# Kernel tuning notes

Measured on AMD Instinct MI355X. Metric: run time of the kernel, lower is better.

The kernel has to match this reference:

```python
import jax, jax.numpy as jnp
import numpy as np

NUM_HEADS = 16
NUM_KV_HEADS = 4
HEAD_DIM = 128
WINDOW = 1024  # sliding window: key j visible to query i iff 0 <= i - j <= WINDOW
SCALE = 0.08838834764831845  # 1/sqrt(HEAD_DIM)
NEG_INF = -1e30


def setup_inputs() -> dict:
    key = jax.random.key(0)
    k1, k2, k3, k4 = jax.random.split(key, 4)
    B, S = 4, 2048
    T = B * S
    return {
        "q": jax.random.normal(k1, (T, NUM_HEADS * HEAD_DIM), dtype=jnp.float32),
        "k": jax.random.normal(k2, (T, NUM_KV_HEADS * HEAD_DIM), dtype=jnp.float32),
        "v": jax.random.normal(k3, (T, NUM_KV_HEADS * HEAD_DIM), dtype=jnp.float32),
        "sinks": jax.random.normal(k4, (NUM_HEADS,), dtype=jnp.float32),
        "batch": B,
        "seqlen": S,
    }


def reference(q, k, v, sinks, batch, seqlen):
    """Varlen causal sliding-window attention with learnable per-head sink logits.

    Equal-length sequences: total_tokens = batch * seqlen, matching
    cu_seqlens = [0, S, 2S, ...] in flash_attn_varlen_func.
    """
    B, S = batch, seqlen
    g = NUM_HEADS // NUM_KV_HEADS
    q = q.reshape(B, S, NUM_HEADS, HEAD_DIM)
    k = k.reshape(B, S, NUM_KV_HEADS, HEAD_DIM)
    v = v.reshape(B, S, NUM_KV_HEADS, HEAD_DIM)
    # GQA: expand kv heads to match query heads
    k = jnp.repeat(k, g, axis=2)  # [B,S,H,D]
    v = jnp.repeat(v, g, axis=2)

    logits = jnp.einsum("bqhd,bkhd->bhqk", q, k) * SCALE  # [B,H,S,S]

    i = jnp.arange(S)[:, None]
    j = jnp.arange(S)[None, :]
    mask = (j <= i) & ((i - j) <= WINDOW)  # causal + sliding window (left=WINDOW, right=-1)
    logits = jnp.where(mask, logits, NEG_INF)

    # Learnable sink: one extra virtual logit per head, contributing no value.
    sink_col = jnp.broadcast_to(sinks[None, :, None, None], (B, NUM_HEADS, S, 1))
    logits = jnp.concatenate([logits, sink_col], axis=-1)  # [B,H,S,S+1]
    probs = jax.nn.softmax(logits, axis=-1)[..., :S]  # drop sink prob (value = 0)

    o = jnp.einsum("bhqk,bkhd->bqhd", probs, v)  # [B,S,H,D]
    return o.reshape(B * S, NUM_HEADS * HEAD_DIM)
```

## Files before the change

### kernel.cpp

```cpp
#include <hip/hip_runtime.h>
#include <hip/hip_bf16.h>

#define NH    16
#define NKVH  4
#define HD    128
#define WIN   1024
#define SEQ   2048
#define NB    4
#define QROW  (NH * HD)
#define KROW  (NKVH * HD)
#define LOG2E 1.4426950408889634f
#define QSC   (0.08838834764831845f * LOG2E)
#define DTHR  8.0f

#define KSTR 136
#define VSTR 40

typedef __attribute__((ext_vector_type(8))) short short8;
typedef __attribute__((ext_vector_type(4))) float float4v;

__device__ __forceinline__ unsigned short f2bf(float f) {
    unsigned int u = __float_as_uint(f);
    unsigned int r = (u + 0x7FFFu + ((u >> 16) & 1u)) >> 16;
    return (unsigned short)r;
}

__device__ __forceinline__ unsigned int pk2bf(float a, float b) {
    float2 t; t.x = a; t.y = b;
    __hip_bfloat162 h = __float22bfloat162_rn(t);
    union { __hip_bfloat162 h; unsigned int u; } cv;
    cv.h = h;
    return cv.u;
}

__global__ __launch_bounds__(256)
void cvt_k_kernel(const float* __restrict__ kg, unsigned short* __restrict__ kb) {
    const size_t idx = ((size_t)blockIdx.x * 256 + threadIdx.x) * 8;
    float4 a = *(const float4*)(kg + idx);
    float4 b = *(const float4*)(kg + idx + 4);
    uint4 w;
    w.x = pk2bf(a.x, a.y); w.y = pk2bf(a.z, a.w);
    w.z = pk2bf(b.x, b.y); w.w = pk2bf(b.z, b.w);
    *(uint4*)(kb + idx) = w;
}

#define VTSTR 72
__global__ __launch_bounds__(256)
void cvt_vt_kernel(const float* __restrict__ vg, unsigned short* __restrict__ vt) {
    __shared__ unsigned short T[128 * VTSTR];
    const int blk = blockIdx.x;
    const int b   = blk >> 7;
    const int kvh = (blk >> 5) & 3;
    const int kb  = blk & 31;
    const int t   = threadIdx.x;

    const int klocal = t >> 2;
    const int d0     = (t & 3) * 32;
    const float* src = vg + (size_t)(b * SEQ + kb * 64 + klocal) * KROW + kvh * HD + d0;
#pragma unroll
    for (int c = 0; c < 8; ++c) {
        float4 x = *(const float4*)(src + c * 4);
        T[(d0 + c * 4 + 0) * VTSTR + klocal] = f2bf(x.x);
        T[(d0 + c * 4 + 1) * VTSTR + klocal] = f2bf(x.y);
        T[(d0 + c * 4 + 2) * VTSTR + klocal] = f2bf(x.z);
        T[(d0 + c * 4 + 3) * VTSTR + klocal] = f2bf(x.w);
    }
    __syncthreads();

    const int d    = t >> 1;
    const int half = t & 1;
    const unsigned short* s = &T[d * VTSTR + half * 32];
    unsigned short* dst = vt + ((size_t)((b * NKVH + kvh) * HD) + d) * SEQ + kb * 64 + half * 32;
#pragma unroll
    for (int c = 0; c < 4; ++c)
        *(uint4*)(dst + c * 8) = *(const uint4*)(s + c * 8);
}

__global__ __launch_bounds__(256, 3)
void attn_swa_sink_kernel(const float* __restrict__ qg,
                          const unsigned short* __restrict__ kb,
                          const unsigned short* __restrict__ vt,
                          const float* __restrict__ sinks,
                          float* __restrict__ og) {
    __shared__ __align__(16) unsigned short Klds[2][32 * KSTR];
    __shared__ __align__(16) unsigned short Vlds[2][128 * VSTR];

    const int gid  = blockIdx.x;
    const int xcd  = gid & 7;
    const int rest = gid >> 3;
    const int qt   = 63 - (rest >> 1);
    const int g    = ((rest & 1) << 3) | xcd;
    const int b    = g >> 2;
    const int kvh  = g & 3;

    const int tid  = threadIdx.x;
    const int wave = tid >> 6;
    const int lane = tid & 63;
    const int l15  = lane & 15;
    const int quad = lane >> 4;
    const int h    = kvh * 4 + wave;
    const int q0   = qt * 32;

    const float* qbase = qg + (size_t)(b * SEQ) * QROW;
    const unsigned short* kbase = kb + (size_t)(b * SEQ) * KROW + kvh * HD;
    const unsigned short* vtbase = vt + (size_t)((b * NKVH + kvh) * HD) * SEQ;

    short8 qf[2][4];
#pragma unroll
    for (int qs = 0; qs < 2; ++qs) {
        const float* qr = qbase + (size_t)(q0 + qs * 16 + l15) * QROW + h * HD + quad * 8;
#pragma unroll
        for (int c = 0; c < 4; ++c) {
            float4 x = *(const float4*)(qr + c * 32);
            float4 y = *(const float4*)(qr + c * 32 + 4);
            union { unsigned int u[4]; short8 s; } cv;
            cv.u[0] = pk2bf(x.x * QSC, x.y * QSC);
            cv.u[1] = pk2bf(x.z * QSC, x.w * QSC);
            cv.u[2] = pk2bf(y.x * QSC, y.y * QSC);
            cv.u[3] = pk2bf(y.z * QSC, y.w * QSC);
            qf[qs][c] = cv.s;
        }
    }

    const float sinkv = sinks[h] * LOG2E;
    float m_i[2] = { sinkv, sinkv };
    float l_i[2] = { 0.0f, 0.0f };
    float4v accO[2][8];
#pragma unroll
    for (int qs = 0; qs < 2; ++qs)
#pragma unroll
        for (int f = 0; f < 8; ++f) accO[qs][f] = (float4v)0.0f;

    const int kr  = tid >> 3, kcg = tid & 7;
    const int lrow = ((kr & 1) << 4) | (kr >> 1);
    const int vd  = tid >> 1, vh = tid & 1;

    int kt0 = q0 - WIN; if (kt0 < 0) kt0 = 0;
    const int kend = q0 + 32;

    const int koff = lrow * KSTR + kcg * 16;
    const int voff = vd * VSTR + vh * 16;

    uint4 kpre0, kpre1, vpre0, vpre1;
    {
        const unsigned short* kp = kbase + (size_t)(kt0 + kr) * KROW + kcg * 16;
        kpre0 = *(const uint4*)(kp);
        kpre1 = *(const uint4*)(kp + 8);
        const unsigned short* vp = vtbase + (size_t)vd * SEQ + kt0 + vh * 16;
        vpre0 = *(const uint4*)(vp);
        vpre1 = *(const uint4*)(vp + 8);
    }

    int pp = 0;
    for (int k0 = kt0; k0 < kend; k0 += 32, pp ^= 1) {
        *(uint4*)&Klds[pp][koff]     = kpre0;
        *(uint4*)&Klds[pp][koff + 8] = kpre1;
        *(uint4*)&Vlds[pp][voff]     = vpre0;
        *(uint4*)&Vlds[pp][voff + 8] = vpre1;
        __syncthreads();
        if (k0 + 32 < kend) {
            const unsigned short* kp = kbase + (size_t)(k0 + 32 + kr) * KROW + kcg * 16;
            kpre0 = *(const uint4*)(kp);
            kpre1 = *(const uint4*)(kp + 8);
            const unsigned short* vp = vtbase + (size_t)vd * SEQ + (k0 + 32) + vh * 16;
            vpre0 = *(const uint4*)(vp);
            vpre1 = *(const uint4*)(vp + 8);
        }

        float4v sacc[2][2];
        sacc[0][0] = (float4v)0.0f; sacc[0][1] = (float4v)0.0f;
        sacc[1][0] = (float4v)0.0f; sacc[1][1] = (float4v)0.0f;
        __builtin_amdgcn_s_setprio(1);
#pragma unroll
        for (int c = 0; c < 4; ++c) {
            short8 kf0 = *(const short8*)&Klds[pp][(l15)      * KSTR + c * 32 + quad * 8];
            short8 kf1 = *(const short8*)&Klds[pp][(16 + l15) * KSTR + c * 32 + quad * 8];
            sacc[0][0] = __builtin_amdgcn_mfma_f32_16x16x32_bf16(kf0, qf[0][c], sacc[0][0], 0, 0, 0);
            sacc[0][1] = __builtin_amdgcn_mfma_f32_16x16x32_bf16(kf0, qf[1][c], sacc[0][1], 0, 0, 0);
            sacc[1][0] = __builtin_amdgcn_mfma_f32_16x16x32_bf16(kf1, qf[0][c], sacc[1][0], 0, 0, 0);
            sacc[1][1] = __builtin_amdgcn_mfma_f32_16x16x32_bf16(kf1, qf[1][c], sacc[1][1], 0, 0, 0);
        }
        __builtin_amdgcn_s_setprio(0);

        short8 pf[2];
#pragma unroll
        for (int qs = 0; qs < 2; ++qs) {
            const int query = q0 + qs * 16 + l15;
            const bool full = (k0 + 31 <= q0 + qs * 16) && (q0 + qs * 16 + 15 - k0 <= WIN);
            float ps[2][4];
            float mx = -3.0e38f;
            if (full) {
#pragma unroll
                for (int ks = 0; ks < 2; ++ks)
#pragma unroll
                    for (int r = 0; r < 4; ++r) {
                        float s = sacc[ks][qs][r];
                        ps[ks][r] = s;
                        mx = fmaxf(mx, s);
                    }
            } else {
#pragma unroll
                for (int ks = 0; ks < 2; ++ks)
#pragma unroll
                    for (int r = 0; r < 4; ++r) {
                        const int key = k0 + 8 * quad + 2 * r + ks;
                        const unsigned d = (unsigned)(query - key);
                        float s = (d <= WIN) ? sacc[ks][qs][r] : -1.0e30f;
                        ps[ks][r] = s;
                        mx = fmaxf(mx, s);
                    }
            }
            mx = fmaxf(mx, __shfl_xor(mx, 16));
            mx = fmaxf(mx, __shfl_xor(mx, 32));
            const float mold = m_i[qs];
            float mnew = mold;
            if (__any(mx > mold + DTHR)) {
                mnew = fmaxf(mold, mx);
                m_i[qs] = mnew;
                const float alpha = exp2f(mold - mnew);
                l_i[qs] *= alpha;
#pragma unroll
                for (int r = 0; r < 4; ++r) {
                    const float ar = __shfl(alpha, quad * 4 + r);
#pragma unroll
                    for (int f = 0; f < 8; ++f) accO[qs][f][r] *= ar;
                }
            }
            float sum = 0.0f;
            union { unsigned int u[4]; short8 s; } cv;
#pragma unroll
            for (int r = 0; r < 4; ++r) {
                const float p0 = exp2f(ps[0][r] - mnew);
                const float p1 = exp2f(ps[1][r] - mnew);
                sum += p0 + p1;
                cv.u[r] = pk2bf(p0, p1);
            }
            l_i[qs] += sum;
            pf[qs] = cv.s;
        }

        __builtin_amdgcn_s_setprio(1);
#pragma unroll
        for (int f = 0; f < 8; ++f) {
            short8 vf = *(const short8*)&Vlds[pp][(f * 16 + l15) * VSTR + quad * 8];
            accO[0][f] = __builtin_amdgcn_mfma_f32_16x16x32_bf16(pf[0], vf, accO[0][f], 0, 0, 0);
            accO[1][f] = __builtin_amdgcn_mfma_f32_16x16x32_bf16(pf[1], vf, accO[1][f], 0, 0, 0);
        }
        __builtin_amdgcn_s_setprio(0);
    }

    float* obase = og + (size_t)(b * SEQ) * QROW + h * HD;
#pragma unroll
    for (int qs = 0; qs < 2; ++qs) {
        float l = l_i[qs];
        l += __shfl_xor(l, 16);
        l += __shfl_xor(l, 32);
        l += exp2f(sinkv - m_i[qs]);
#pragma unroll
        for (int r = 0; r < 4; ++r) {
            const float lq  = __shfl(l, quad * 4 + r);
            const float inv = __builtin_amdgcn_rcpf(lq);
            float* orow = obase + (size_t)(q0 + qs * 16 + quad * 4 + r) * QROW;
#pragma unroll
            for (int f = 0; f < 8; ++f)
                orow[f * 16 + l15] = accO[qs][f][r] * inv;
        }
    }
}

extern "C" void kernel_launch(void* const* d_in, const int* in_sizes, int n_in,
                              void* d_out, int out_size, void* d_ws, size_t ws_size,
                              hipStream_t stream) {
    const float* q     = (const float*)d_in[0];
    const float* k     = (const float*)d_in[1];
    const float* v     = (const float*)d_in[2];
    const float* sinks = (const float*)d_in[3];
    float* o = (float*)d_out;

    unsigned short* kb = (unsigned short*)d_ws;
    unsigned short* vt = kb + (size_t)NB * SEQ * KROW;

    cvt_k_kernel<<<dim3(NB * SEQ * KROW / (256 * 8)), dim3(256), 0, stream>>>(k, kb);
    cvt_vt_kernel<<<dim3(NB * NKVH * (SEQ / 64)), dim3(256), 0, stream>>>(v, vt);

    attn_swa_sink_kernel<<<dim3(NB * NKVH * (SEQ / 32)), dim3(256), 0, stream>>>(
        q, kb, vt, sinks, o);
}
```

Baseline: 225.0 us.

## Share K/V tiles across two query sub-tiles with 512-thread blocks

Each block now covers 64 queries with 8 waves instead of 32 queries with 4 waves. The two wave groups share one staged K/V tile stream, and each group skips key tiles outside its own window range. Every thread now loads one uint4 per K and V tile instead of two. This halves the number of blocks and roughly halves global K/V traffic per query. In exchange, idle waves still hit the barriers on the tiles they skip, which causes some imbalance, and 512-thread blocks with launch bounds of 3 may put more pressure on registers.

```diff
diff --git a/kernel.cpp b/kernel.cpp
--- a/kernel.cpp
+++ b/kernel.cpp
@@ -76,7 +76,7 @@
         *(uint4*)(dst + c * 8) = *(const uint4*)(s + c * 8);
 }
 
-__global__ __launch_bounds__(256, 3)
+__global__ __launch_bounds__(512, 3)
 void attn_swa_sink_kernel(const float* __restrict__ qg,
                           const unsigned short* __restrict__ kb,
                           const unsigned short* __restrict__ vt,
@@ -88,18 +88,19 @@
     const int gid  = blockIdx.x;
     const int xcd  = gid & 7;
     const int rest = gid >> 3;
-    const int qt   = 63 - (rest >> 1);
+    const int qt   = 31 - (rest >> 1);
     const int g    = ((rest & 1) << 3) | xcd;
     const int b    = g >> 2;
     const int kvh  = g & 3;
 
-    const int tid  = threadIdx.x;
-    const int wave = tid >> 6;
-    const int lane = tid & 63;
-    const int l15  = lane & 15;
-    const int quad = lane >> 4;
-    const int h    = kvh * 4 + wave;
-    const int q0   = qt * 32;
+    const int tid   = threadIdx.x;
+    const int wave  = tid >> 6;
+    const int lane  = tid & 63;
+    const int l15   = lane & 15;
+    const int quad  = lane >> 4;
+    const int qhalf = wave >> 2;
+    const int h     = kvh * 4 + (wave & 3);
+    const int qw    = qt * 64 + qhalf * 32;
 
     const float* qbase = qg + (size_t)(b * SEQ) * QROW;
     const unsigned short* kbase = kb + (size_t)(b * SEQ) * KROW + kvh * HD;
@@ -108,7 +109,7 @@
     short8 qf[2][4];
 #pragma unroll
     for (int qs = 0; qs < 2; ++qs) {
-        const float* qr = qbase + (size_t)(q0 + qs * 16 + l15) * QROW + h * HD + quad * 8;
+        const float* qr = qbase + (size_t)(qw + qs * 16 + l15) * QROW + h * HD + quad * 8;
 #pragma unroll
         for (int c = 0; c < 4; ++c) {
             float4 x = *(const float4*)(qr + c * 32);
@@ -131,41 +132,37 @@
 #pragma unroll
         for (int f = 0; f < 8; ++f) accO[qs][f] = (float4v)0.0f;
 
-    const int kr  = tid >> 3, kcg = tid & 7;
+    const int q0 = qt * 64;
+    int kt0 = q0 - WIN; if (kt0 < 0) kt0 = 0;
+    const int kend = q0 + 64;
+
+    const int cstart = kt0 + ((qhalf == 1 && q0 + 32 - WIN > kt0) ? 32 : 0);
+    const int cend   = (qhalf == 0) ? (qw + 32) : kend;
+
+    const int kr  = tid >> 4, kcg = tid & 15;
     const int lrow = ((kr & 1) << 4) | (kr >> 1);
-    const int vd  = tid >> 1, vh = tid & 1;
-
-    int kt0 = q0 - WIN; if (kt0 < 0) kt0 = 0;
-    const int kend = q0 + 32;
-
-    const int koff = lrow * KSTR + kcg * 16;
-    const int voff = vd * VSTR + vh * 16;
-
-    uint4 kpre0, kpre1, vpre0, vpre1;
+    const int vd  = tid >> 2, vh = tid & 3;
+
+    const int koff = lrow * KSTR + kcg * 8;
+    const int voff = vd * VSTR + vh * 8;
+
+    uint4 kpre, vpre;
     {
-        const unsigned short* kp = kbase + (size_t)(kt0 + kr) * KROW + kcg * 16;
-        kpre0 = *(const uint4*)(kp);
-        kpre1 = *(const uint4*)(kp + 8);
-        const unsigned short* vp = vtbase + (size_t)vd * SEQ + kt0 + vh * 16;
-        vpre0 = *(const uint4*)(vp);
-        vpre1 = *(const uint4*)(vp + 8);
+        kpre = *(const uint4*)(kbase + (size_t)(kt0 + kr) * KROW + kcg * 8);
+        vpre = *(const uint4*)(vtbase + (size_t)vd * SEQ + kt0 + vh * 8);
     }
 
     int pp = 0;
     for (int k0 = kt0; k0 < kend; k0 += 32, pp ^= 1) {
-        *(uint4*)&Klds[pp][koff]     = kpre0;
-        *(uint4*)&Klds[pp][koff + 8] = kpre1;
-        *(uint4*)&Vlds[pp][voff]     = vpre0;
-        *(uint4*)&Vlds[pp][voff + 8] = vpre1;
+        *(uint4*)&Klds[pp][koff] = kpre;
+        *(uint4*)&Vlds[pp][voff] = vpre;
         __syncthreads();
         if (k0 + 32 < kend) {
-            const unsigned short* kp = kbase + (size_t)(k0 + 32 + kr) * KROW + kcg * 16;
-            kpre0 = *(const uint4*)(kp);
-            kpre1 = *(const uint4*)(kp + 8);
-            const unsigned short* vp = vtbase + (size_t)vd * SEQ + (k0 + 32) + vh * 16;
-            vpre0 = *(const uint4*)(vp);
-            vpre1 = *(const uint4*)(vp + 8);
-        }
+            kpre = *(const uint4*)(kbase + (size_t)(k0 + 32 + kr) * KROW + kcg * 8);
+            vpre = *(const uint4*)(vtbase + (size_t)vd * SEQ + (k0 + 32) + vh * 8);
+        }
+
+        if (k0 < cstart || k0 >= cend) continue;
 
         float4v sacc[2][2];
         sacc[0][0] = (float4v)0.0f; sacc[0][1] = (float4v)0.0f;
@@ -185,8 +182,8 @@
         short8 pf[2];
 #pragma unroll
         for (int qs = 0; qs < 2; ++qs) {
-            const int query = q0 + qs * 16 + l15;
-            const bool full = (k0 + 31 <= q0 + qs * 16) && (q0 + qs * 16 + 15 - k0 <= WIN);
+            const int query = qw + qs * 16 + l15;
+            const bool full = (k0 + 31 <= qw + qs * 16) && (qw + qs * 16 + 15 - k0 <= WIN);
             float ps[2][4];
             float mx = -3.0e38f;
             if (full) {
@@ -260,7 +257,7 @@
         for (int r = 0; r < 4; ++r) {
             const float lq  = __shfl(l, quad * 4 + r);
             const float inv = __builtin_amdgcn_rcpf(lq);
-            float* orow = obase + (size_t)(q0 + qs * 16 + quad * 4 + r) * QROW;
+            float* orow = obase + (size_t)(qw + qs * 16 + quad * 4 + r) * QROW;
 #pragma unroll
             for (int f = 0; f < 8; ++f)
                 orow[f * 16 + l15] = accO[qs][f][r] * inv;
@@ -283,6 +280,6 @@
     cvt_k_kernel<<<dim3(NB * SEQ * KROW / (256 * 8)), dim3(256), 0, stream>>>(k, kb);
     cvt_vt_kernel<<<dim3(NB * NKVH * (SEQ / 64)), dim3(256), 0, stream>>>(v, vt);
 
-    attn_swa_sink_kernel<<<dim3(NB * NKVH * (SEQ / 32)), dim3(256), 0, stream>>>(
+    attn_swa_sink_kernel<<<dim3(NB * NKVH * (SEQ / 64)), dim3(512), 0, stream>>>(
         q, kb, vt, sinks, o);
 }
```

Result: slower. 256.8 us (+14.2%).
